# Kernel tuning notes

Hardware: AMD Instinct MI355X
Metric: run time of the kernel (lower is better)

The kernel has to match this reference:

```python
import jax, jax.numpy as jnp
import numpy as np

N_CLOSEST = 16
OBJECTNESS_THRESH = 0.75


def _masked_softmax(att, mask):
    # softmax over axis 1 restricted to mask; rows with empty mask -> all zeros
    neg = jnp.where(mask, att, -jnp.inf)
    m = jnp.max(neg, axis=1, keepdims=True)
    m = jnp.where(jnp.isfinite(m), m, 0.0)
    e = jnp.where(mask, jnp.exp(att - m), 0.0)
    d = jnp.sum(e, axis=1, keepdims=True)
    return jnp.where(d > 0, e / jnp.maximum(d, 1e-30), 0.0)


def _forward(aggregated_vote_features, ref_obj_features, objectness_scores,
             ref_center_label, aggregated_vote_xyz, emb_table, init_emb,
             W_enc_att, b_enc_att, W_dec_att, b_dec_att, w_full_att, b_full_att,
             W_ih, b_ih, W_hh, b_hh, W_init_h, b_init_h, W_init_c, b_init_c,
             W_fbeta, b_fbeta, W_fc, b_fc, lang_indices, lang_len):
    B, K, VD = aggregated_vote_features.shape
    T = lang_indices.shape[1]

    # --- objectness + distance (top-k closest) masking ---
    objness = jax.nn.softmax(objectness_scores, axis=-1)[:, :, -1]      # [B,K]
    omask = objness > OBJECTNESS_THRESH
    dist = jnp.linalg.norm(ref_center_label[:, None, :] - aggregated_vote_xyz, axis=2)
    dist = jnp.where(omask, dist, jnp.inf)
    closest = -jax.lax.top_k(-dist, N_CLOSEST)[0]                        # k smallest
    max_d = jnp.max(closest, axis=1, keepdims=True)
    object_mask = omask & (dist <= max_d)                                # [B,K]

    enc = aggregated_vote_features                                       # [B,K,VD]
    init_in = jnp.concatenate([enc.mean(axis=1), ref_obj_features], axis=1)
    h0 = init_in @ W_init_h.T + b_init_h                                 # [B,D]
    c0 = init_in @ W_init_c.T + b_init_c

    # encoder attention projection is constant over timesteps
    att1 = jnp.einsum('bkv,av->bka', enc, W_enc_att) + b_enc_att         # [B,K,A]

    # teacher-forcing inputs: <unk> init embedding then caption embeddings
    E = init_emb.shape[-1]
    emb = jnp.concatenate(
        [jnp.broadcast_to(init_emb, (B, E))[:, None, :], emb_table[lang_indices]],
        axis=1)                                                          # [B,T+1,E]
    emb_steps = jnp.swapaxes(emb[:, :T], 0, 1)                           # [T,B,E]
    t_steps = jnp.arange(T)

    def step(carry, xs):
        h, c = carry
        emb_t, t = xs
        # attention
        att2 = h @ W_dec_att.T + b_dec_att                               # [B,A]
        att = jax.nn.relu(att1 + att2[:, None, :]) @ w_full_att + b_full_att[0]  # [B,K]
        alpha = _masked_softmax(att, object_mask)
        awe = jnp.einsum('bkv,bk->bv', enc, alpha)                       # [B,VD]
        gate = jax.nn.sigmoid(h @ W_fbeta.T + b_fbeta)
        awe = gate * awe
        # LSTMCell (torch gate order i,f,g,o)
        x = jnp.concatenate([emb_t, awe, ref_obj_features], axis=1)      # [B,E+VD+OD]
        gates = x @ W_ih.T + b_ih + h @ W_hh.T + b_hh
        i, f, g, o = jnp.split(gates, 4, axis=1)
        c_new = jax.nn.sigmoid(f) * c + jax.nn.sigmoid(i) * jnp.tanh(g)
        h_new = jax.nn.sigmoid(o) * jnp.tanh(c_new)
        # only samples with length > t are decoded (masked equivalent of batch_size_t)
        active = (t < lang_len)[:, None]
        preds = jnp.where(active, h_new @ W_fc.T + b_fc, 0.0)            # [B,V]
        alpha_o = jnp.where(active, alpha, 0.0)
        h = jnp.where(active, h_new, h)
        c = jnp.where(active, c_new, c)
        return (h, c), (preds, alpha_o)

    _, (preds_seq, alpha_seq) = jax.lax.scan(step, (h0, c0), (emb_steps, t_steps))
    predictions = jnp.transpose(preds_seq, (1, 2, 0))                    # [B,V,T]
    alphas = jnp.transpose(alpha_seq, (1, 0, 2))                         # [B,T,K]
    return predictions, alphas, object_mask


def setup_inputs() -> dict:
    key = jax.random.key(0)
    ks = jax.random.split(key, 20)
    B, K, VD, OD, E, A, D, V, T = 128, 128, 128, 256, 300, 512, 512, 4000, 32
    ENC = VD + OD

    def rn(k, shape, s=1.0):
        return jax.random.normal(k, shape, jnp.float32) * s

    return {
        'aggregated_vote_features': rn(ks[0], (B, K, VD)),
        'ref_obj_features': rn(ks[1], (B, OD)),
        'objectness_scores': rn(ks[2], (B, K, 2)),
        'ref_center_label': rn(ks[3], (B, 3)),
        'aggregated_vote_xyz': rn(ks[4], (B, K, 3)),
        'lang_indices': jax.random.randint(ks[5], (B, T), 0, V),
        'lang_len': jax.random.randint(ks[6], (B,), 1, T + 1),
        'emb_table': rn(ks[7], (V, E), 0.1),
        'init_emb': rn(ks[8], (1, E), 0.1),
        'W_enc_att': rn(ks[9], (A, VD), 0.05), 'b_enc_att': jnp.zeros((A,)),
        'W_dec_att': rn(ks[10], (A, D), 0.05), 'b_dec_att': jnp.zeros((A,)),
        'w_full_att': rn(ks[11], (A,), 0.05), 'b_full_att': jnp.zeros((1,)),
        'W_ih': rn(ks[12], (4 * D, E + ENC), 0.05), 'b_ih': jnp.zeros((4 * D,)),
        'W_hh': rn(ks[13], (4 * D, D), 0.05), 'b_hh': jnp.zeros((4 * D,)),
        'W_init_h': rn(ks[14], (D, ENC), 0.05), 'b_init_h': jnp.zeros((D,)),
        'W_init_c': rn(ks[15], (D, ENC), 0.05), 'b_init_c': jnp.zeros((D,)),
        'W_fbeta': rn(ks[16], (VD, D), 0.05), 'b_fbeta': jnp.zeros((VD,)),
        'W_fc': rn(ks[17], (V, D), 0.1), 'b_fc': jnp.zeros((V,)),
    }


def reference(aggregated_vote_features, ref_obj_features, objectness_scores,
              ref_center_label, aggregated_vote_xyz, lang_indices, lang_len,
              emb_table, init_emb, W_enc_att, b_enc_att, W_dec_att, b_dec_att,
              w_full_att, b_full_att, W_ih, b_ih, W_hh, b_hh, W_init_h, b_init_h,
              W_init_c, b_init_c, W_fbeta, b_fbeta, W_fc, b_fc):
    return _forward(aggregated_vote_features, ref_obj_features, objectness_scores,
                    ref_center_label, aggregated_vote_xyz, emb_table, init_emb,
                    W_enc_att, b_enc_att, W_dec_att, b_dec_att, w_full_att, b_full_att,
                    W_ih, b_ih, W_hh, b_hh, W_init_h, b_init_h, W_init_c, b_init_c,
                    W_fbeta, b_fbeta, W_fc, b_fc, lang_indices, lang_len)
```

## Files before the change

### kernel.cpp

```cpp
#include <hip/hip_runtime.h>
#include <hip/hip_bf16.h>
#include <math.h>

#define XKTOT 1196
#define XKP   1216

typedef unsigned short u16;
typedef short bf16x8 __attribute__((ext_vector_type(8)));
typedef float f32x4 __attribute__((ext_vector_type(4)));

static __device__ __forceinline__ float sigmoidf_(float x){ return 1.f/(1.f+expf(-x)); }
static __device__ __forceinline__ u16 f2bf(float x){ __hip_bfloat16 h = __float2bfloat16(x); return *reinterpret_cast<u16*>(&h); }
static __device__ __forceinline__ float bf2f(u16 u){ __hip_bfloat16 h; *reinterpret_cast<u16*>(&h) = u; return __bfloat162float(h); }

__global__ __launch_bounds__(256) void k_transpose(const float* __restrict__ in,
                                                   float* __restrict__ out, int R, int C) {
  __shared__ float tile[32][33];
  int c0 = blockIdx.x * 32, r0 = blockIdx.y * 32;
  int tx = threadIdx.x & 31, ty = threadIdx.x >> 5;
  for (int i = 0; i < 32; i += 8) {
    int r = r0 + ty + i, c = c0 + tx;
    tile[ty + i][tx] = (r < R && c < C) ? in[(size_t)r * C + c] : 0.f;
  }
  __syncthreads();
  for (int i = 0; i < 32; i += 8) {
    int c = c0 + ty + i, r = r0 + tx;
    if (c < C && r < R) out[(size_t)c * R + r] = tile[tx][ty + i];
  }
}

__global__ __launch_bounds__(256) void k_cvt(const float* __restrict__ in,
                                             u16* __restrict__ out, int n) {
  for (int i = blockIdx.x * 256 + threadIdx.x; i < n; i += gridDim.x * 256)
    out[i] = f2bf(in[i]);
}

__global__ __launch_bounds__(256) void k_wcat_split(const float* __restrict__ W_ih,
                                                    const float* __restrict__ W_hh,
                                                    u16* __restrict__ Whi,
                                                    u16* __restrict__ Wlo) {
  int np = blockIdx.x;
  int d = np >> 2, g = np & 3;
  int j = g * 512 + d;
  for (int c = threadIdx.x; c < XKP; c += 256) {
    float v;
    if (c < 684)        v = W_ih[(size_t)j * 684 + c];
    else if (c < 1196)  v = W_hh[(size_t)j * 512 + (c - 684)];
    else                v = 0.f;
    u16 hi = f2bf(v);
    u16 lo = f2bf(v - bf2f(hi));
    Whi[(size_t)np * XKP + c] = hi;
    Wlo[(size_t)np * XKP + c] = lo;
  }
}

__global__ __launch_bounds__(128) void k_mask(const float* __restrict__ objs,
                                              const float* __restrict__ rcl,
                                              const float* __restrict__ avx,
                                              const float* __restrict__ enc,
                                              float* __restrict__ maskf,
                                              float* __restrict__ encmean,
                                              float* __restrict__ out_mask) {
  int b = blockIdx.x, k = threadIdx.x;
  __shared__ float dsh[128];
  __shared__ float maxd;
  float s0 = objs[(size_t)(b * 128 + k) * 2 + 0];
  float s1 = objs[(size_t)(b * 128 + k) * 2 + 1];
  float mx = fmaxf(s0, s1);
  float e0 = expf(s0 - mx), e1 = expf(s1 - mx);
  float p  = e1 / (e0 + e1);
  bool om  = p > 0.75f;
  float dx = rcl[b * 3 + 0] - avx[(size_t)(b * 128 + k) * 3 + 0];
  float dy = rcl[b * 3 + 1] - avx[(size_t)(b * 128 + k) * 3 + 1];
  float dz = rcl[b * 3 + 2] - avx[(size_t)(b * 128 + k) * 3 + 2];
  float dist = sqrtf(dx * dx + dy * dy + dz * dz);
  float dm = om ? dist : INFINITY;
  dsh[k] = dm;
  __syncthreads();
  float v = dm; int clt = 0, cle = 0;
  for (int j = 0; j < 128; j++) { float o = dsh[j]; clt += (o < v); cle += (o <= v); }
  if (clt < 16 && cle >= 16) maxd = v;
  __syncthreads();
  bool msk = om && (dm <= maxd);
  maskf[b * 128 + k]    = msk ? 1.f : 0.f;
  out_mask[b * 128 + k] = msk ? 1.f : 0.f;
  float s = 0.f;
  for (int kk = 0; kk < 128; kk++) s += enc[(size_t)(b * 128 + kk) * 128 + k];
  encmean[b * 128 + k] = s * (1.f / 128.f);
}

__global__ __launch_bounds__(512) void k_init(const float* __restrict__ encm,
                                              const float* __restrict__ rof,
                                              const float* __restrict__ wihT,
                                              const float* __restrict__ wicT,
                                              const float* __restrict__ bh,
                                              const float* __restrict__ bc,
                                              float* __restrict__ h, float* __restrict__ c,
                                              u16* __restrict__ hb16) {
  int b = blockIdx.x, d = threadIdx.x;
  __shared__ float xin[384];
  if (d < 128) xin[d] = encm[b * 128 + d];
  else if (d < 384) xin[d] = rof[(size_t)b * 256 + (d - 128)];
  __syncthreads();
  float ah = bh[d], ac = bc[d];
  for (int i = 0; i < 384; i++) {
    float x = xin[i];
    ah += x * wihT[(size_t)i * 512 + d];
    ac += x * wicT[(size_t)i * 512 + d];
  }
  size_t idx = (size_t)b * 512 + d;
  h[idx] = ah;
  c[idx] = ac;
  hb16[idx] = f2bf(ah);
}

__global__ __launch_bounds__(256) void k_att1m(const u16* __restrict__ enc16,
                                               const u16* __restrict__ We16,
                                               const float* __restrict__ b_enc,
                                               float* __restrict__ att1) {
  int w = threadIdx.x >> 6, lane = threadIdx.x & 63;
  int gw = blockIdx.x * 4 + w;
  int nt = gw & 15, mt = gw >> 4;
  int m0 = mt * 32, n0 = nt * 32;
  int rc = lane & 15, kb = lane >> 4;
  const bf16x8* a0 = (const bf16x8*)(enc16 + (size_t)(m0 + rc) * 128) + kb;
  const bf16x8* a1 = (const bf16x8*)(enc16 + (size_t)(m0 + 16 + rc) * 128) + kb;
  const bf16x8* b0 = (const bf16x8*)(We16 + (size_t)(n0 + rc) * 128) + kb;
  const bf16x8* b1 = (const bf16x8*)(We16 + (size_t)(n0 + 16 + rc) * 128) + kb;
  f32x4 z = {0.f, 0.f, 0.f, 0.f};
  f32x4 acc00 = z, acc01 = z, acc10 = z, acc11 = z;
#pragma unroll
  for (int kk = 0; kk < 4; kk++) {
    bf16x8 av0 = a0[kk * 4], av1 = a1[kk * 4];
    bf16x8 bv0 = b0[kk * 4], bv1 = b1[kk * 4];
    acc00 = __builtin_amdgcn_mfma_f32_16x16x32_bf16(av0, bv0, acc00, 0, 0, 0);
    acc01 = __builtin_amdgcn_mfma_f32_16x16x32_bf16(av0, bv1, acc01, 0, 0, 0);
    acc10 = __builtin_amdgcn_mfma_f32_16x16x32_bf16(av1, bv0, acc10, 0, 0, 0);
    acc11 = __builtin_amdgcn_mfma_f32_16x16x32_bf16(av1, bv1, acc11, 0, 0, 0);
  }
  int col = lane & 15, rbase = (lane >> 4) * 4;
#pragma unroll
  for (int r = 0; r < 4; r++) {
    int r0g = m0 + rbase + r;
    att1[(size_t)r0g * 512 + n0 + col]        = acc00[r] + b_enc[n0 + col];
    att1[(size_t)r0g * 512 + n0 + 16 + col]   = acc01[r] + b_enc[n0 + 16 + col];
    att1[(size_t)(r0g + 16) * 512 + n0 + col]      = acc10[r] + b_enc[n0 + col];
    att1[(size_t)(r0g + 16) * 512 + n0 + 16 + col] = acc11[r] + b_enc[n0 + 16 + col];
  }
}

__global__ __launch_bounds__(512) void k_step_att(
    const float* __restrict__ att1, const float* __restrict__ h,
    const float* __restrict__ wdT, const float* __restrict__ b_dec,
    const float* __restrict__ wfull, const float* __restrict__ bfull,
    const float* __restrict__ enc, const float* __restrict__ maskf,
    const float* __restrict__ wfbT, const float* __restrict__ b_fbeta,
    const float* __restrict__ rof, const float* __restrict__ embt,
    const float* __restrict__ iemb, const int* __restrict__ lidx,
    const int* __restrict__ llen, u16* __restrict__ Xhi, u16* __restrict__ Xlo,
    float* __restrict__ alphas_out, int t) {
  int b = blockIdx.x, tid = threadIdx.x;
  __shared__ float hs[512], att2[512], wf[512], attk[128], alph[128], awes[128];
  __shared__ float red1[2], red2[2];
  hs[tid] = h[(size_t)b * 512 + tid];
  wf[tid] = wfull[tid];
  __syncthreads();
  {
    float acc = b_dec[tid];
    for (int i = 0; i < 512; i++) acc += hs[i] * wdT[(size_t)i * 512 + tid];
    att2[tid] = acc;
  }
  __syncthreads();
  int k = tid >> 2, j = tid & 3;
  {
    const float4* a1 = (const float4*)(att1 + (size_t)(b * 128 + k) * 512 + j * 128);
    float s = 0.f;
#pragma unroll 4
    for (int i = 0; i < 32; i++) {
      float4 v = a1[i];
      int base = j * 128 + i * 4;
      s += fmaxf(v.x + att2[base + 0], 0.f) * wf[base + 0];
      s += fmaxf(v.y + att2[base + 1], 0.f) * wf[base + 1];
      s += fmaxf(v.z + att2[base + 2], 0.f) * wf[base + 2];
      s += fmaxf(v.w + att2[base + 3], 0.f) * wf[base + 3];
    }
    s += __shfl_xor(s, 1);
    s += __shfl_xor(s, 2);
    if (j == 0) attk[k] = s + bfull[0];
  }
  __syncthreads();
  float mk = 0.f, av = 0.f;
  if (tid < 128) { mk = maskf[b * 128 + tid]; av = attk[tid]; }
  float nv = (tid < 128 && mk != 0.f) ? av : -INFINITY;
  float wm = nv;
#pragma unroll
  for (int o = 32; o > 0; o >>= 1) wm = fmaxf(wm, __shfl_xor(wm, o));
  if (tid < 128 && (tid & 63) == 0) red1[tid >> 6] = wm;
  __syncthreads();
  float m = fmaxf(red1[0], red1[1]);
  float e = 0.f;
  if (tid < 128 && mk != 0.f) e = expf(av - m);
  float sred = e;
#pragma unroll
  for (int o = 32; o > 0; o >>= 1) sred += __shfl_xor(sred, o);
  if (tid < 128 && (tid & 63) == 0) red2[tid >> 6] = sred;
  __syncthreads();
  float dsum = red2[0] + red2[1];
  float alpha = (dsum > 0.f) ? e / fmaxf(dsum, 1e-30f) : 0.f;
  int active = t < llen[b];
  if (tid < 128) {
    alph[tid] = alpha;
    alphas_out[(size_t)(b * 32 + t) * 128 + tid] = active ? alpha : 0.f;
  }
  __syncthreads();
  float awe_v = 0.f;
  if (tid < 128) {
    for (int kk = 0; kk < 128; kk++)
      awe_v += alph[kk] * enc[(size_t)(b * 128 + kk) * 128 + tid];
  }
  {
    int v = tid >> 2;
    float g = 0.f;
    for (int ii = 0; ii < 128; ii++) {
      int i = j * 128 + ii;
      g += hs[i] * wfbT[(size_t)i * 128 + v];
    }
    g += __shfl_xor(g, 1);
    g += __shfl_xor(g, 2);
    if (j == 0) attk[v] = sigmoidf_(g + b_fbeta[v]);
  }
  __syncthreads();
  if (tid < 128) awes[tid] = awe_v * attk[tid];
  __syncthreads();
  const float* esrc = (t == 0) ? iemb : (embt + (size_t)lidx[b * 32 + (t - 1)] * 300);
  for (int c = tid; c < XKP; c += 512) {
    float val;
    if (c < 300)       val = esrc[c];
    else if (c < 428)  val = awes[c - 300];
    else if (c < 684)  val = rof[(size_t)b * 256 + (c - 428)];
    else if (c < 1196) val = hs[c - 684];
    else               val = 0.f;
    u16 hi = f2bf(val);
    Xhi[(size_t)b * XKP + c] = hi;
    Xlo[(size_t)b * XKP + c] = f2bf(val - bf2f(hi));
  }
}

__global__ __launch_bounds__(256) void k_gates(const u16* __restrict__ Xhi,
                                               const u16* __restrict__ Xlo,
                                               const u16* __restrict__ Whi,
                                               const u16* __restrict__ Wlo,
                                               const float* __restrict__ b_ih,
                                               const float* __restrict__ b_hh,
                                               const int* __restrict__ llen,
                                               float* __restrict__ h, float* __restrict__ c,
                                               u16* __restrict__ hb16, int t) {
  int w = threadIdx.x >> 6, lane = threadIdx.x & 63;
  int mt = blockIdx.x >> 5;
  int nt = (blockIdx.x & 31) * 4 + w;
  int m0 = mt * 16, n0 = nt * 16;
  int rc = lane & 15, kb = lane >> 4;
  const bf16x8* aHi = (const bf16x8*)(Xhi + (size_t)(m0 + rc) * XKP) + kb;
  const bf16x8* aLo = (const bf16x8*)(Xlo + (size_t)(m0 + rc) * XKP) + kb;
  const bf16x8* bHi = (const bf16x8*)(Whi + (size_t)(n0 + rc) * XKP) + kb;
  const bf16x8* bLo = (const bf16x8*)(Wlo + (size_t)(n0 + rc) * XKP) + kb;
  f32x4 acc = {0.f, 0.f, 0.f, 0.f};
#pragma unroll 2
  for (int kk = 0; kk < 38; kk++) {
    bf16x8 ah = aHi[kk * 4], al = aLo[kk * 4];
    bf16x8 bh = bHi[kk * 4], bl = bLo[kk * 4];
    acc = __builtin_amdgcn_mfma_f32_16x16x32_bf16(ah, bh, acc, 0, 0, 0);
    acc = __builtin_amdgcn_mfma_f32_16x16x32_bf16(al, bh, acc, 0, 0, 0);
    acc = __builtin_amdgcn_mfma_f32_16x16x32_bf16(ah, bl, acc, 0, 0, 0);
  }
  __shared__ float tile[4][16][17];
#pragma unroll
  for (int r = 0; r < 4; r++) tile[w][(lane >> 4) * 4 + r][lane & 15] = acc[r];
  __syncthreads();
  int lb = lane & 15, ld = lane >> 4;
  int b = m0 + lb, d = nt * 4 + ld;
  if (t < llen[b]) {
    float g4[4];
#pragma unroll
    for (int g = 0; g < 4; g++) {
      int jj = g * 512 + d;
      g4[g] = tile[w][lb][ld * 4 + g] + b_ih[jj] + b_hh[jj];
    }
    float i_ = sigmoidf_(g4[0]);
    float f_ = sigmoidf_(g4[1]);
    float gg = tanhf(g4[2]);
    float o_ = sigmoidf_(g4[3]);
    size_t idx = (size_t)b * 512 + d;
    float cn = f_ * c[idx] + i_ * gg;
    float hn = o_ * tanhf(cn);
    c[idx] = cn;
    h[idx] = hn;
    hb16[idx] = f2bf(hn);
  }
}

__global__ __launch_bounds__(256) void k_fc(const u16* __restrict__ hb16,
                                            const u16* __restrict__ Wfc16,
                                            const float* __restrict__ b_fc,
                                            const int* __restrict__ llen,
                                            float* __restrict__ dst, int t, int direct) {
  int w = threadIdx.x >> 6, lane = threadIdx.x & 63;
  int gw = blockIdx.x * 4 + w;
  int mt = gw & 7, nt = gw >> 3;
  int m0 = mt * 16, n0 = nt * 16;
  int rc = lane & 15, kb = lane >> 4;
  const bf16x8* aP = (const bf16x8*)(hb16 + (size_t)(m0 + rc) * 512) + kb;
  const bf16x8* bP = (const bf16x8*)(Wfc16 + (size_t)(n0 + rc) * 512) + kb;
  f32x4 acc = {0.f, 0.f, 0.f, 0.f};
#pragma unroll 4
  for (int kk = 0; kk < 16; kk++)
    acc = __builtin_amdgcn_mfma_f32_16x16x32_bf16(aP[kk * 4], bP[kk * 4], acc, 0, 0, 0);
  int col = lane & 15, rbase = (lane >> 4) * 4;
  int v = n0 + col;
  float bias = b_fc[v];
#pragma unroll
  for (int r = 0; r < 4; r++) {
    int b = m0 + rbase + r;
    float val = (t < llen[b]) ? (acc[r] + bias) : 0.f;
    if (direct) dst[((size_t)b * 4000 + v) * 32 + t] = val;
    else        dst[((size_t)(t * 128 + b)) * 4000 + v] = val;
  }
}

__global__ __launch_bounds__(256) void k_out_tr(const float* __restrict__ predsT,
                                                float* __restrict__ out) {
  __shared__ float tile[32][33];
  int b = blockIdx.y, v0 = blockIdx.x * 32;
  int tx = threadIdx.x & 31, ty = threadIdx.x >> 5;
  for (int i = 0; i < 32; i += 8) {
    int tt = ty + i;
    tile[tt][tx] = predsT[((size_t)tt * 128 + b) * 4000 + v0 + tx];
  }
  __syncthreads();
  for (int i = 0; i < 32; i += 8) {
    int v = v0 + ty + i;
    out[((size_t)b * 4000 + v) * 32 + tx] = tile[tx][ty + i];
  }
}

extern "C" void kernel_launch(void* const* d_in, const int* in_sizes, int n_in,
                              void* d_out, int out_size, void* d_ws, size_t ws_size,
                              hipStream_t stream) {
  (void)in_sizes; (void)n_in; (void)out_size;
  const float* avf   = (const float*)d_in[0];
  const float* rof   = (const float*)d_in[1];
  const float* objs  = (const float*)d_in[2];
  const float* rcl   = (const float*)d_in[3];
  const float* avx   = (const float*)d_in[4];
  const int*   lidx  = (const int*)d_in[5];
  const int*   llen  = (const int*)d_in[6];
  const float* embt  = (const float*)d_in[7];
  const float* iemb  = (const float*)d_in[8];
  const float* W_enc = (const float*)d_in[9];
  const float* b_enc = (const float*)d_in[10];
  const float* W_dec = (const float*)d_in[11];
  const float* b_dec = (const float*)d_in[12];
  const float* wfull = (const float*)d_in[13];
  const float* bfull = (const float*)d_in[14];
  const float* W_ih  = (const float*)d_in[15];
  const float* b_ih  = (const float*)d_in[16];
  const float* W_hh  = (const float*)d_in[17];
  const float* b_hh  = (const float*)d_in[18];
  const float* W_inh = (const float*)d_in[19];
  const float* b_inh = (const float*)d_in[20];
  const float* W_inc = (const float*)d_in[21];
  const float* b_inc = (const float*)d_in[22];
  const float* W_fb  = (const float*)d_in[23];
  const float* b_fb  = (const float*)d_in[24];
  const float* W_fc  = (const float*)d_in[25];
  const float* b_fc  = (const float*)d_in[26];

  float* ws = (float*)d_ws;
  size_t f = 0;
  auto A8 = [&](size_t n) { size_t o = f; f += (n + 63) & ~(size_t)63; return o; };
  float* att1  = ws + A8((size_t)128 * 128 * 512);
  float* wdT   = ws + A8(512 * 512);
  float* wihT  = ws + A8(384 * 512);
  float* wicT  = ws + A8(384 * 512);
  float* wfbT  = ws + A8(512 * 128);
  float* hbuf  = ws + A8(128 * 512);
  float* cbuf  = ws + A8(128 * 512);
  float* maskf = ws + A8(128 * 128);
  float* encm  = ws + A8(128 * 128);
  u16*   Xhi   = (u16*)(ws + A8((size_t)128 * XKP / 2));
  u16*   Xlo   = (u16*)(ws + A8((size_t)128 * XKP / 2));
  u16*   WcatHi= (u16*)(ws + A8((size_t)2048 * XKP / 2));
  u16*   WcatLo= (u16*)(ws + A8((size_t)2048 * XKP / 2));
  u16*   enc16 = (u16*)(ws + A8((size_t)128 * 128 * 128 / 2));
  u16*   We16  = (u16*)(ws + A8((size_t)512 * 128 / 2));
  u16*   Wfc16 = (u16*)(ws + A8((size_t)4000 * 512 / 2));
  u16*   hb16  = (u16*)(ws + A8((size_t)128 * 512 / 2));
  float* predsT= ws + A8((size_t)32 * 128 * 4000);
  bool useT = ws_size >= f * sizeof(float);

  float* out_pred  = (float*)d_out;
  float* out_alpha = out_pred + (size_t)16384000;
  float* out_mask  = out_alpha + (size_t)524288;

  k_transpose<<<dim3(16, 16), 256, 0, stream>>>(W_dec, wdT, 512, 512);
  k_transpose<<<dim3(12, 16), 256, 0, stream>>>(W_inh, wihT, 512, 384);
  k_transpose<<<dim3(12, 16), 256, 0, stream>>>(W_inc, wicT, 512, 384);
  k_transpose<<<dim3(16, 4),  256, 0, stream>>>(W_fb, wfbT, 128, 512);
  k_wcat_split<<<2048, 256, 0, stream>>>(W_ih, W_hh, WcatHi, WcatLo);
  k_cvt<<<2048, 256, 0, stream>>>(avf, enc16, 128 * 128 * 128);
  k_cvt<<<256,  256, 0, stream>>>(W_enc, We16, 512 * 128);
  k_cvt<<<2048, 256, 0, stream>>>(W_fc, Wfc16, 4000 * 512);
  k_mask<<<128, 128, 0, stream>>>(objs, rcl, avx, avf, maskf, encm, out_mask);
  k_init<<<128, 512, 0, stream>>>(encm, rof, wihT, wicT, b_inh, b_inc, hbuf, cbuf, hb16);
  k_att1m<<<2048, 256, 0, stream>>>(enc16, We16, b_enc, att1);

  for (int t = 0; t < 32; t++) {
    k_step_att<<<128, 512, 0, stream>>>(att1, hbuf, wdT, b_dec, wfull, bfull,
        avf, maskf, wfbT, b_fb, rof, embt, iemb, lidx, llen, Xhi, Xlo, out_alpha, t);
    k_gates<<<256, 256, 0, stream>>>(Xhi, Xlo, WcatHi, WcatLo, b_ih, b_hh, llen,
                                     hbuf, cbuf, hb16, t);
    k_fc<<<500, 256, 0, stream>>>(hb16, Wfc16, b_fc, llen,
                                  useT ? predsT : out_pred, t, useT ? 0 : 1);
  }
  if (useT) k_out_tr<<<dim3(125, 128), 256, 0, stream>>>(predsT, out_pred);
}
```

Baseline: 2.435 ms.

## Defer vocab projection to one batched GEMM and store attention inputs in bf16

The per-timestep FC kernel is removed. Each step's hidden state is now written as bf16 into a [T*B,512] buffer, and a single large MFMA GEMM after the recurrence produces all predictions at once. This cuts 32 small launches and reuses the W_fc tiles across timesteps. The step kernel also reads the precomputed encoder attention projection and the encoder features as bf16 instead of fp32, which halves that memory traffic. The gate epilogue now uses lane shuffles instead of LDS. Storing the attention projection in bf16 adds rounding error to the attention scores.

```diff
diff --git a/kernel.cpp b/kernel.cpp
--- a/kernel.cpp
+++ b/kernel.cpp
@@ -2,16 +2,17 @@
 #include <hip/hip_bf16.h>
 #include <math.h>
 
-#define XKTOT 1196
-#define XKP   1216
+#define XKP 1216
 
 typedef unsigned short u16;
 typedef short bf16x8 __attribute__((ext_vector_type(8)));
+typedef u16 ushort8 __attribute__((ext_vector_type(8)));
 typedef float f32x4 __attribute__((ext_vector_type(4)));
 
 static __device__ __forceinline__ float sigmoidf_(float x){ return 1.f/(1.f+expf(-x)); }
 static __device__ __forceinline__ u16 f2bf(float x){ __hip_bfloat16 h = __float2bfloat16(x); return *reinterpret_cast<u16*>(&h); }
 static __device__ __forceinline__ float bf2f(u16 u){ __hip_bfloat16 h; *reinterpret_cast<u16*>(&h) = u; return __bfloat162float(h); }
+static __device__ __forceinline__ float bfb(u16 u){ return __uint_as_float(((unsigned)u) << 16); }
 
 __global__ __launch_bounds__(256) void k_transpose(const float* __restrict__ in,
                                                    float* __restrict__ out, int R, int C) {
@@ -95,8 +96,7 @@
                                               const float* __restrict__ wicT,
                                               const float* __restrict__ bh,
                                               const float* __restrict__ bc,
-                                              float* __restrict__ h, float* __restrict__ c,
-                                              u16* __restrict__ hb16) {
+                                              float* __restrict__ h, float* __restrict__ c) {
   int b = blockIdx.x, d = threadIdx.x;
   __shared__ float xin[384];
   if (d < 128) xin[d] = encm[b * 128 + d];
@@ -111,13 +111,12 @@
   size_t idx = (size_t)b * 512 + d;
   h[idx] = ah;
   c[idx] = ac;
-  hb16[idx] = f2bf(ah);
 }
 
 __global__ __launch_bounds__(256) void k_att1m(const u16* __restrict__ enc16,
                                                const u16* __restrict__ We16,
                                                const float* __restrict__ b_enc,
-                                               float* __restrict__ att1) {
+                                               u16* __restrict__ att1b) {
   int w = threadIdx.x >> 6, lane = threadIdx.x & 63;
   int gw = blockIdx.x * 4 + w;
   int nt = gw & 15, mt = gw >> 4;
@@ -142,47 +141,56 @@
 #pragma unroll
   for (int r = 0; r < 4; r++) {
     int r0g = m0 + rbase + r;
-    att1[(size_t)r0g * 512 + n0 + col]        = acc00[r] + b_enc[n0 + col];
-    att1[(size_t)r0g * 512 + n0 + 16 + col]   = acc01[r] + b_enc[n0 + 16 + col];
-    att1[(size_t)(r0g + 16) * 512 + n0 + col]      = acc10[r] + b_enc[n0 + col];
-    att1[(size_t)(r0g + 16) * 512 + n0 + 16 + col] = acc11[r] + b_enc[n0 + 16 + col];
-  }
-}
-
-__global__ __launch_bounds__(512) void k_step_att(
-    const float* __restrict__ att1, const float* __restrict__ h,
+    att1b[(size_t)r0g * 512 + n0 + col]             = f2bf(acc00[r] + b_enc[n0 + col]);
+    att1b[(size_t)r0g * 512 + n0 + 16 + col]        = f2bf(acc01[r] + b_enc[n0 + 16 + col]);
+    att1b[(size_t)(r0g + 16) * 512 + n0 + col]      = f2bf(acc10[r] + b_enc[n0 + col]);
+    att1b[(size_t)(r0g + 16) * 512 + n0 + 16 + col] = f2bf(acc11[r] + b_enc[n0 + 16 + col]);
+  }
+}
+
+__global__ __launch_bounds__(512) void k_step(
+    const u16* __restrict__ att1b, const float* __restrict__ hbuf,
     const float* __restrict__ wdT, const float* __restrict__ b_dec,
     const float* __restrict__ wfull, const float* __restrict__ bfull,
-    const float* __restrict__ enc, const float* __restrict__ maskf,
-    const float* __restrict__ wfbT, const float* __restrict__ b_fbeta,
+    const u16* __restrict__ enc16, const float* __restrict__ maskf,
+    const float* __restrict__ wfbT, const float* __restrict__ b_fb,
     const float* __restrict__ rof, const float* __restrict__ embt,
     const float* __restrict__ iemb, const int* __restrict__ lidx,
     const int* __restrict__ llen, u16* __restrict__ Xhi, u16* __restrict__ Xlo,
     float* __restrict__ alphas_out, int t) {
-  int b = blockIdx.x, tid = threadIdx.x;
-  __shared__ float hs[512], att2[512], wf[512], attk[128], alph[128], awes[128];
-  __shared__ float red1[2], red2[2];
-  hs[tid] = h[(size_t)b * 512 + tid];
+  const int tid = threadIdx.x;
+  const int w = tid >> 6, lane = tid & 63;
+  const int b = blockIdx.x;
+
+  __shared__ float hs[512], a2s[512], wf[512];
+  __shared__ float attk[128], alph[128], awes[128];
+  __shared__ float red1[8], red2[8];
+
+  hs[tid] = hbuf[(size_t)b * 512 + tid];
   wf[tid] = wfull[tid];
   __syncthreads();
   {
-    float acc = b_dec[tid];
-    for (int i = 0; i < 512; i++) acc += hs[i] * wdT[(size_t)i * 512 + tid];
-    att2[tid] = acc;
+    float ac0 = 0.f, ac1 = 0.f, ac2 = 0.f, ac3 = 0.f;
+    for (int i = 0; i < 512; i += 4) {
+      ac0 += hs[i + 0] * wdT[(size_t)(i + 0) * 512 + tid];
+      ac1 += hs[i + 1] * wdT[(size_t)(i + 1) * 512 + tid];
+      ac2 += hs[i + 2] * wdT[(size_t)(i + 2) * 512 + tid];
+      ac3 += hs[i + 3] * wdT[(size_t)(i + 3) * 512 + tid];
+    }
+    a2s[tid] = (ac0 + ac1) + (ac2 + ac3) + b_dec[tid];
   }
   __syncthreads();
   int k = tid >> 2, j = tid & 3;
   {
-    const float4* a1 = (const float4*)(att1 + (size_t)(b * 128 + k) * 512 + j * 128);
+    const ushort8* a1 = (const ushort8*)(att1b + (size_t)(b * 128 + k) * 512 + j * 128);
     float s = 0.f;
-#pragma unroll 4
-    for (int i = 0; i < 32; i++) {
-      float4 v = a1[i];
-      int base = j * 128 + i * 4;
-      s += fmaxf(v.x + att2[base + 0], 0.f) * wf[base + 0];
-      s += fmaxf(v.y + att2[base + 1], 0.f) * wf[base + 1];
-      s += fmaxf(v.z + att2[base + 2], 0.f) * wf[base + 2];
-      s += fmaxf(v.w + att2[base + 3], 0.f) * wf[base + 3];
+#pragma unroll 2
+    for (int i = 0; i < 16; i++) {
+      ushort8 v = a1[i];
+      int base = j * 128 + i * 8;
+#pragma unroll
+      for (int e = 0; e < 8; e++)
+        s += fmaxf(bfb(v[e]) + a2s[base + e], 0.f) * wf[base + e];
     }
     s += __shfl_xor(s, 1);
     s += __shfl_xor(s, 2);
@@ -195,15 +203,14 @@
   float wm = nv;
 #pragma unroll
   for (int o = 32; o > 0; o >>= 1) wm = fmaxf(wm, __shfl_xor(wm, o));
-  if (tid < 128 && (tid & 63) == 0) red1[tid >> 6] = wm;
+  if (tid < 128 && lane == 0) red1[w] = wm;
   __syncthreads();
   float m = fmaxf(red1[0], red1[1]);
-  float e = 0.f;
-  if (tid < 128 && mk != 0.f) e = expf(av - m);
-  float sred = e;
-#pragma unroll
-  for (int o = 32; o > 0; o >>= 1) sred += __shfl_xor(sred, o);
-  if (tid < 128 && (tid & 63) == 0) red2[tid >> 6] = sred;
+  float e = (tid < 128 && mk != 0.f) ? expf(av - m) : 0.f;
+  float sr = e;
+#pragma unroll
+  for (int o = 32; o > 0; o >>= 1) sr += __shfl_xor(sr, o);
+  if (tid < 128 && lane == 0) red2[w] = sr;
   __syncthreads();
   float dsum = red2[0] + red2[1];
   float alpha = (dsum > 0.f) ? e / fmaxf(dsum, 1e-30f) : 0.f;
@@ -213,11 +220,6 @@
     alphas_out[(size_t)(b * 32 + t) * 128 + tid] = active ? alpha : 0.f;
   }
   __syncthreads();
-  float awe_v = 0.f;
-  if (tid < 128) {
-    for (int kk = 0; kk < 128; kk++)
-      awe_v += alph[kk] * enc[(size_t)(b * 128 + kk) * 128 + tid];
-  }
   {
     int v = tid >> 2;
     float g = 0.f;
@@ -227,10 +229,14 @@
     }
     g += __shfl_xor(g, 1);
     g += __shfl_xor(g, 2);
-    if (j == 0) attk[v] = sigmoidf_(g + b_fbeta[v]);
-  }
-  __syncthreads();
-  if (tid < 128) awes[tid] = awe_v * attk[tid];
+    float gate = sigmoidf_(g + b_fb[v]);
+    float aw = 0.f;
+    for (int kk = j * 32; kk < j * 32 + 32; kk++)
+      aw += alph[kk] * bfb(enc16[(size_t)(b * 128 + kk) * 128 + v]);
+    aw += __shfl_xor(aw, 1);
+    aw += __shfl_xor(aw, 2);
+    if (j == 0) awes[v] = aw * gate;
+  }
   __syncthreads();
   const float* esrc = (t == 0) ? iemb : (embt + (size_t)lidx[b * 32 + (t - 1)] * 300);
   for (int c = tid; c < XKP; c += 512) {
@@ -246,24 +252,25 @@
   }
 }
 
-__global__ __launch_bounds__(256) void k_gates(const u16* __restrict__ Xhi,
-                                               const u16* __restrict__ Xlo,
-                                               const u16* __restrict__ Whi,
-                                               const u16* __restrict__ Wlo,
-                                               const float* __restrict__ b_ih,
-                                               const float* __restrict__ b_hh,
-                                               const int* __restrict__ llen,
-                                               float* __restrict__ h, float* __restrict__ c,
-                                               u16* __restrict__ hb16, int t) {
-  int w = threadIdx.x >> 6, lane = threadIdx.x & 63;
-  int mt = blockIdx.x >> 5;
-  int nt = (blockIdx.x & 31) * 4 + w;
-  int m0 = mt * 16, n0 = nt * 16;
-  int rc = lane & 15, kb = lane >> 4;
+__global__ __launch_bounds__(256) void k_gates2(const u16* __restrict__ Xhi,
+                                                const u16* __restrict__ Xlo,
+                                                const u16* __restrict__ WcatHi,
+                                                const u16* __restrict__ WcatLo,
+                                                const float* __restrict__ b_ih,
+                                                const float* __restrict__ b_hh,
+                                                const int* __restrict__ llen,
+                                                float* __restrict__ hbuf,
+                                                float* __restrict__ cbuf,
+                                                u16* __restrict__ hball, int t) {
+  const int w = threadIdx.x >> 6, lane = threadIdx.x & 63;
+  const int rc = lane & 15, kb = lane >> 4;
+  const int np = blockIdx.x >> 1;
+  const int mg = (blockIdx.x & 1) * 4 + w;
+  int m0 = mg * 16, n0 = np * 16;
   const bf16x8* aHi = (const bf16x8*)(Xhi + (size_t)(m0 + rc) * XKP) + kb;
   const bf16x8* aLo = (const bf16x8*)(Xlo + (size_t)(m0 + rc) * XKP) + kb;
-  const bf16x8* bHi = (const bf16x8*)(Whi + (size_t)(n0 + rc) * XKP) + kb;
-  const bf16x8* bLo = (const bf16x8*)(Wlo + (size_t)(n0 + rc) * XKP) + kb;
+  const bf16x8* bHi = (const bf16x8*)(WcatHi + (size_t)(n0 + rc) * XKP) + kb;
+  const bf16x8* bLo = (const bf16x8*)(WcatLo + (size_t)(n0 + rc) * XKP) + kb;
   f32x4 acc = {0.f, 0.f, 0.f, 0.f};
 #pragma unroll 2
   for (int kk = 0; kk < 38; kk++) {
@@ -273,57 +280,61 @@
     acc = __builtin_amdgcn_mfma_f32_16x16x32_bf16(al, bh, acc, 0, 0, 0);
     acc = __builtin_amdgcn_mfma_f32_16x16x32_bf16(ah, bl, acc, 0, 0, 0);
   }
-  __shared__ float tile[4][16][17];
-#pragma unroll
-  for (int r = 0; r < 4; r++) tile[w][(lane >> 4) * 4 + r][lane & 15] = acc[r];
-  __syncthreads();
-  int lb = lane & 15, ld = lane >> 4;
-  int b = m0 + lb, d = nt * 4 + ld;
-  if (t < llen[b]) {
-    float g4[4];
-#pragma unroll
-    for (int g = 0; g < 4; g++) {
-      int jj = g * 512 + d;
-      g4[g] = tile[w][lb][ld * 4 + g] + b_ih[jj] + b_hh[jj];
+  int col = lane & 15;
+  int d = np * 4 + (col >> 2);
+  int baseL = lane & ~3;
+#pragma unroll
+  for (int r = 0; r < 4; r++) {
+    int bb = m0 + (lane >> 4) * 4 + r;
+    float g0 = __shfl(acc[r], baseL + 0);
+    float g1 = __shfl(acc[r], baseL + 1);
+    float g2 = __shfl(acc[r], baseL + 2);
+    float g3 = __shfl(acc[r], baseL + 3);
+    if ((lane & 3) == 0 && t < llen[bb]) {
+      float i_ = sigmoidf_(g0 + b_ih[d]        + b_hh[d]);
+      float f_ = sigmoidf_(g1 + b_ih[512 + d]  + b_hh[512 + d]);
+      float gg = tanhf   (g2 + b_ih[1024 + d] + b_hh[1024 + d]);
+      float o_ = sigmoidf_(g3 + b_ih[1536 + d] + b_hh[1536 + d]);
+      size_t idx = (size_t)bb * 512 + d;
+      float cn = f_ * cbuf[idx] + i_ * gg;
+      float hn = o_ * tanhf(cn);
+      cbuf[idx] = cn;
+      hbuf[idx] = hn;
+      hball[((size_t)t * 128 + bb) * 512 + d] = f2bf(hn);
     }
-    float i_ = sigmoidf_(g4[0]);
-    float f_ = sigmoidf_(g4[1]);
-    float gg = tanhf(g4[2]);
-    float o_ = sigmoidf_(g4[3]);
-    size_t idx = (size_t)b * 512 + d;
-    float cn = f_ * c[idx] + i_ * gg;
-    float hn = o_ * tanhf(cn);
-    c[idx] = cn;
-    h[idx] = hn;
-    hb16[idx] = f2bf(hn);
-  }
-}
-
-__global__ __launch_bounds__(256) void k_fc(const u16* __restrict__ hb16,
-                                            const u16* __restrict__ Wfc16,
-                                            const float* __restrict__ b_fc,
-                                            const int* __restrict__ llen,
-                                            float* __restrict__ dst, int t, int direct) {
-  int w = threadIdx.x >> 6, lane = threadIdx.x & 63;
-  int gw = blockIdx.x * 4 + w;
-  int mt = gw & 7, nt = gw >> 3;
-  int m0 = mt * 16, n0 = nt * 16;
-  int rc = lane & 15, kb = lane >> 4;
-  const bf16x8* aP = (const bf16x8*)(hb16 + (size_t)(m0 + rc) * 512) + kb;
+  }
+}
+
+__global__ __launch_bounds__(256) void k_fc_def(const u16* __restrict__ hball,
+                                                const u16* __restrict__ Wfc16,
+                                                const float* __restrict__ b_fc,
+                                                const int* __restrict__ llen,
+                                                float* __restrict__ dst, int direct) {
+  const int w = threadIdx.x >> 6, lane = threadIdx.x & 63;
+  const int rc = lane & 15, kb = lane >> 4;
+  int nb = blockIdx.x;
+  int n0 = nb * 16;
   const bf16x8* bP = (const bf16x8*)(Wfc16 + (size_t)(n0 + rc) * 512) + kb;
-  f32x4 acc = {0.f, 0.f, 0.f, 0.f};
-#pragma unroll 4
-  for (int kk = 0; kk < 16; kk++)
-    acc = __builtin_amdgcn_mfma_f32_16x16x32_bf16(aP[kk * 4], bP[kk * 4], acc, 0, 0, 0);
-  int col = lane & 15, rbase = (lane >> 4) * 4;
-  int v = n0 + col;
-  float bias = b_fc[v];
-#pragma unroll
-  for (int r = 0; r < 4; r++) {
-    int b = m0 + rbase + r;
-    float val = (t < llen[b]) ? (acc[r] + bias) : 0.f;
-    if (direct) dst[((size_t)b * 4000 + v) * 32 + t] = val;
-    else        dst[((size_t)(t * 128 + b)) * 4000 + v] = val;
+#pragma unroll
+  for (int s = 0; s < 2; s++) {
+    int mtile = blockIdx.y * 8 + w * 2 + s;
+    int m0 = mtile * 16;
+    const bf16x8* aP = (const bf16x8*)(hball + (size_t)(m0 + rc) * 512) + kb;
+    f32x4 acc = {0.f, 0.f, 0.f, 0.f};
+#pragma unroll
+    for (int kk = 0; kk < 16; kk++)
+      acc = __builtin_amdgcn_mfma_f32_16x16x32_bf16(aP[kk * 4], bP[kk * 4], acc, 0, 0, 0);
+    int col = lane & 15, rb = (lane >> 4) * 4;
+    int v = n0 + col;
+    float bias = b_fc[v];
+#pragma unroll
+    for (int r = 0; r < 4; r++) {
+      int gr = m0 + rb + r;
+      int t = gr >> 7, bb = gr & 127;
+      float val = (t < llen[bb]) ? (acc[r] + bias) : 0.f;
+      if (direct) dst[((size_t)bb * 4000 + v) * 32 + t] = val;
+      else        dst[(size_t)gr * 4000 + v] = val;
+    }
   }
 }
 
@@ -378,7 +389,7 @@
   float* ws = (float*)d_ws;
   size_t f = 0;
   auto A8 = [&](size_t n) { size_t o = f; f += (n + 63) & ~(size_t)63; return o; };
-  float* att1  = ws + A8((size_t)128 * 128 * 512);
+  u16*   att1b = (u16*)(ws + A8((size_t)16384 * 512 / 2));
   float* wdT   = ws + A8(512 * 512);
   float* wihT  = ws + A8(384 * 512);
   float* wicT  = ws + A8(384 * 512);
@@ -394,7 +405,7 @@
   u16*   enc16 = (u16*)(ws + A8((size_t)128 * 128 * 128 / 2));
   u16*   We16  = (u16*)(ws + A8((size_t)512 * 128 / 2));
   u16*   Wfc16 = (u16*)(ws + A8((size_t)4000 * 512 / 2));
-  u16*   hb16  = (u16*)(ws + A8((size_t)128 * 512 / 2));
+  u16*   hball = (u16*)(ws + A8((size_t)32 * 128 * 512 / 2));
   float* predsT= ws + A8((size_t)32 * 128 * 4000);
   bool useT = ws_size >= f * sizeof(float);
 
@@ -411,16 +422,17 @@
   k_cvt<<<256,  256, 0, stream>>>(W_enc, We16, 512 * 128);
   k_cvt<<<2048, 256, 0, stream>>>(W_fc, Wfc16, 4000 * 512);
   k_mask<<<128, 128, 0, stream>>>(objs, rcl, avx, avf, maskf, encm, out_mask);
-  k_init<<<128, 512, 0, stream>>>(encm, rof, wihT, wicT, b_inh, b_inc, hbuf, cbuf, hb16);
-  k_att1m<<<2048, 256, 0, stream>>>(enc16, We16, b_enc, att1);
+  k_init<<<128, 512, 0, stream>>>(encm, rof, wihT, wicT, b_inh, b_inc, hbuf, cbuf);
+  k_att1m<<<2048, 256, 0, stream>>>(enc16, We16, b_enc, att1b);
 
   for (int t = 0; t < 32; t++) {
-    k_step_att<<<128, 512, 0, stream>>>(att1, hbuf, wdT, b_dec, wfull, bfull,
-        avf, maskf, wfbT, b_fb, rof, embt, iemb, lidx, llen, Xhi, Xlo, out_alpha, t);
-    k_gates<<<256, 256, 0, stream>>>(Xhi, Xlo, WcatHi, WcatLo, b_ih, b_hh, llen,
-                                     hbuf, cbuf, hb16, t);
-    k_fc<<<500, 256, 0, stream>>>(hb16, Wfc16, b_fc, llen,
-                                  useT ? predsT : out_pred, t, useT ? 0 : 1);
-  }
+    k_step<<<128, 512, 0, stream>>>(att1b, hbuf, wdT, b_dec, wfull, bfull,
+        enc16, maskf, wfbT, b_fb, rof, embt, iemb, lidx, llen, Xhi, Xlo, out_alpha, t);
+    k_gates2<<<256, 256, 0, stream>>>(Xhi, Xlo, WcatHi, WcatLo, b_ih, b_hh, llen,
+                                      hbuf, cbuf, hball, t);
+  }
+
+  k_fc_def<<<dim3(250, 32), 256, 0, stream>>>(hball, Wfc16, b_fc, llen,
+                                              useT ? predsT : out_pred, useT ? 0 : 1);
   if (useT) k_out_tr<<<dim3(125, 128), 256, 0, stream>>>(predsT, out_pred);
 }
```

Result: faster. 2.276 ms (-6.5%).
